# Optimization experiments

Hardware: AMD Instinct MI355X
Metric: run time of the kernel (lower is better)

The kernel has to match this reference:

```python
import jax, jax.numpy as jnp
import numpy as np

D_MODEL = 1024
N_HEADS = 16
BATCH = 2
SEQ = 2048


def get_freqs(seq, n_dim):
    # standard RoPE frequencies: [seq, n_dim//2]
    inv_freq = 1.0 / (10000.0 ** (jnp.arange(0, n_dim, 2, dtype=jnp.float32) / n_dim))
    return jnp.arange(seq, dtype=jnp.float32)[:, None] * inv_freq[None, :]


def rope(x, freqs):
    # x: [batch, seq, heads, n_dim]; half-split rotation convention
    half = x.shape[-1] // 2
    cos = jnp.cos(freqs)[None, :, None, :]  # [1, seq, 1, half]
    sin = jnp.sin(freqs)[None, :, None, :]
    x1, x2 = x[..., :half], x[..., half:]
    return jnp.concatenate([x1 * cos - x2 * sin, x1 * sin + x2 * cos], axis=-1)


def setup_inputs() -> dict:
    key = jax.random.key(0)
    ks = jax.random.split(key, 5)
    x = jax.random.normal(ks[0], (BATCH, SEQ, D_MODEL), dtype=jnp.float32)
    qw = jax.random.normal(ks[1], (D_MODEL, D_MODEL), dtype=jnp.float32)
    kw = jax.random.normal(ks[2], (D_MODEL, D_MODEL), dtype=jnp.float32)
    vw = jax.random.normal(ks[3], (D_MODEL, D_MODEL), dtype=jnp.float32)
    ow = jax.random.normal(ks[4], (D_MODEL, D_MODEL), dtype=jnp.float32)
    return {"x": x, "qw": qw, "kw": kw, "vw": vw, "ow": ow}


def reference(x, qw, kw, vw, ow):
    batch, seq, dim = x.shape
    n_heads = N_HEADS
    n_dim = dim // n_heads
    Q = (x @ qw).reshape(batch, seq, n_heads, n_dim)
    K = (x @ kw).reshape(batch, seq, n_heads, n_dim)
    V = (x @ vw).reshape(batch, seq, n_heads, n_dim)
    freqs = get_freqs(seq, n_dim)
    Q = rope(Q, freqs)
    K = rope(K, freqs)
    # NOTE: original divides by sqrt(d_model), not sqrt(head_dim)
    scale = 1.0 / jnp.sqrt(jnp.float32(dim))
    score = jnp.einsum('bqhd,bkhd->bhqk', Q, K) * scale
    weights = jax.nn.softmax(score.astype(jnp.float32), axis=-1)
    attn = jnp.einsum('bhqk,bkhd->bqhd', weights, V)
    merged = attn.reshape(batch, seq, dim)
    return merged @ ow
```

## Files before the change

kernel.cpp:

```cpp
#include <hip/hip_runtime.h>
#include <math.h>

#define DM 1024
#define NH 16
#define HD 64
#define BB 2
#define SS 2048
#define MM (BB*SS)

typedef unsigned short ushort_t;
typedef __attribute__((ext_vector_type(8))) short short8;
typedef __attribute__((ext_vector_type(4))) short short4_t;
typedef __attribute__((ext_vector_type(4))) float floatx4;

__device__ __forceinline__ ushort_t f2bf(float f) {
    unsigned int u = __float_as_uint(f);
    unsigned int r = u + 0x7fffu + ((u >> 16) & 1u);
    return (ushort_t)(r >> 16);
}
__device__ __forceinline__ float bf2f(ushort_t h) {
    return __uint_as_float(((unsigned int)h) << 16);
}

__device__ __forceinline__ void gl_lds16(const ushort_t* g, ushort_t* l) {
    __builtin_amdgcn_global_load_lds(
        (const __attribute__((address_space(1))) unsigned int*)g,
        (__attribute__((address_space(3))) unsigned int*)l, 16, 0, 0);
}

__global__ __launch_bounds__(256) void freq_kernel(float2* __restrict__ ct)
{
    const int idx = blockIdx.x * 256 + threadIdx.x;
    const int s = idx >> 5, j = idx & 31;
    const float invf = powf(10000.f, -(float)j * (1.f / 32.f));
    float sn, cs;
    sincosf((float)s * invf, &sn, &cs);
    ct[idx] = make_float2(cs, sn);
}

__global__ __launch_bounds__(256) void convert_x(const float* __restrict__ X,
                                                 ushort_t* __restrict__ Xh,
                                                 ushort_t* __restrict__ Xl)
{
    const size_t base = ((size_t)blockIdx.x * 256 + threadIdx.x) * 8;
    float v[8];
    *(float4*)&v[0] = *(const float4*)(X + base);
    *(float4*)&v[4] = *(const float4*)(X + base + 4);
    short8 h, l;
#pragma unroll
    for (int i = 0; i < 8; ++i) {
        const ushort_t hi = f2bf(v[i]);
        h[i] = (short)hi;
        l[i] = (short)f2bf(v[i] - bf2f(hi));
    }
    *(short8*)(Xh + base) = h;
    *(short8*)(Xl + base) = l;
}

template<int SPLIT>
__global__ __launch_bounds__(256) void convert_wt(const float* __restrict__ W,
                                                  ushort_t* __restrict__ Th,
                                                  ushort_t* __restrict__ Tl)
{
    __shared__ float tile[64][65];
    const int t  = threadIdx.x;
    const int kb = blockIdx.y * 64, nb = blockIdx.x * 64;
    const int r  = t >> 2;
    const int c0 = (t & 3) * 16;
#pragma unroll
    for (int i = 0; i < 4; ++i)
        *(float4*)&tile[r][c0 + 4 * i] = *(const float4*)(W + (size_t)(kb + r) * DM + nb + c0 + 4 * i);
    __syncthreads();
    ushort_t hi[16], lo[16];
#pragma unroll
    for (int i = 0; i < 16; ++i) {
        const float v = tile[c0 + i][r];
        hi[i] = f2bf(v);
        if (SPLIT) lo[i] = f2bf(v - bf2f(hi[i]));
    }
    const size_t dst = (size_t)(nb + r) * DM + kb + c0;
    *(short8*)(Th + dst)     = *(short8*)&hi[0];
    *(short8*)(Th + dst + 8) = *(short8*)&hi[8];
    if (SPLIT) {
        *(short8*)(Tl + dst)     = *(short8*)&lo[0];
        *(short8*)(Tl + dst + 8) = *(short8*)&lo[8];
    }
}

#define GTM 128

template<int UPR, int SH>
__device__ __forceinline__ void stage_tile(const ushort_t* __restrict__ G,
                                           ushort_t* L, int rows, int w, int lane)
{
    const int iters = rows * UPR / 256;
#pragma unroll
    for (int i = 0; i < iters; ++i) {
        const int p0 = (i * 4 + w) * 64;
        const int p  = p0 + lane;
        const int r  = p / UPR;
        const int u  = (p % UPR) ^ ((r >> SH) & (UPR - 1));
        gl_lds16(G + (size_t)r * DM + u * 8, L + (size_t)p0 * 8);
    }
}

template<int UPR, int SH>
__device__ __forceinline__ short8 frag(const ushort_t* L, int r, int u)
{
    const int uu = u ^ ((r >> SH) & (UPR - 1));
    return *(const short8*)&L[((size_t)r * UPR + uu) * 8];
}

template<int SPLIT, int OUT_MODE, int TN, int BK>
__global__ __launch_bounds__(256, 2) void gemm_mfma(
    const ushort_t* __restrict__ Ah, const ushort_t* __restrict__ Al,
    const ushort_t* __restrict__ Bh, const ushort_t* __restrict__ Bl,
    float* __restrict__ Cf, ushort_t* __restrict__ Cb, ushort_t* __restrict__ Cb2,
    const float2* __restrict__ CT)
{
    constexpr int UPR = BK / 8;
    constexpr int KC  = BK / 32;
    constexpr int NI  = TN / 32;
    constexpr int SH  = (UPR == 4) ? 1 : 0;

    __shared__ __align__(16) ushort_t AsH[GTM * BK];
    __shared__ __align__(16) ushort_t BsH[TN * BK];
    __shared__ __align__(16) ushort_t AsL[SPLIT ? GTM * BK : 8];
    __shared__ __align__(16) ushort_t BsL[SPLIT ? TN * BK : 8];
    __shared__ __align__(16) ushort_t Ts[(OUT_MODE == 2) ? 64 * 136 : 8];

    const int t    = threadIdx.x;
    const int w    = t >> 6;
    const int lane = t & 63;
    const int col  = lane & 15;
    const int quad = lane >> 4;
    const int wm   = w & 1;
    const int wn   = w >> 1;
    const int m0   = blockIdx.y * GTM;
    const int n0   = blockIdx.x * TN;

    floatx4 acc[4][NI];
#pragma unroll
    for (int mi = 0; mi < 4; ++mi)
#pragma unroll
        for (int ni = 0; ni < NI; ++ni) acc[mi][ni] = (floatx4){0.f, 0.f, 0.f, 0.f};

    for (int k0 = 0; k0 < DM; k0 += BK) {
        __syncthreads();
        stage_tile<UPR, SH>(Ah + (size_t)m0 * DM + k0, AsH, GTM, w, lane);
        if (SPLIT) stage_tile<UPR, SH>(Al + (size_t)m0 * DM + k0, AsL, GTM, w, lane);
        stage_tile<UPR, SH>(Bh + (size_t)n0 * DM + k0, BsH, TN, w, lane);
        if (SPLIT) stage_tile<UPR, SH>(Bl + (size_t)n0 * DM + k0, BsL, TN, w, lane);
        __syncthreads();

#pragma unroll
        for (int kc = 0; kc < KC; ++kc) {
            short8 ah[4], bh[NI];
            short8 al[SPLIT ? 4 : 1], bl[SPLIT ? NI : 1];
#pragma unroll
            for (int mi = 0; mi < 4; ++mi) {
                const int r = wm * 64 + mi * 16 + col;
                ah[mi] = frag<UPR, SH>(AsH, r, kc * 4 + quad);
                if (SPLIT) al[mi] = frag<UPR, SH>(AsL, r, kc * 4 + quad);
            }
#pragma unroll
            for (int ni = 0; ni < NI; ++ni) {
                const int r = wn * (TN / 2) + ni * 16 + col;
                bh[ni] = frag<UPR, SH>(BsH, r, kc * 4 + quad);
                if (SPLIT) bl[ni] = frag<UPR, SH>(BsL, r, kc * 4 + quad);
            }
#pragma unroll
            for (int mi = 0; mi < 4; ++mi)
#pragma unroll
                for (int ni = 0; ni < NI; ++ni) {
                    acc[mi][ni] = __builtin_amdgcn_mfma_f32_16x16x32_bf16(ah[mi], bh[ni], acc[mi][ni], 0, 0, 0);
                    if (SPLIT) {
                        acc[mi][ni] = __builtin_amdgcn_mfma_f32_16x16x32_bf16(al[mi], bh[ni], acc[mi][ni], 0, 0, 0);
                        acc[mi][ni] = __builtin_amdgcn_mfma_f32_16x16x32_bf16(ah[mi], bl[ni], acc[mi][ni], 0, 0, 0);
                    }
                }
        }
    }

    if constexpr (OUT_MODE == 0) {
#pragma unroll
        for (int mi = 0; mi < 4; ++mi)
#pragma unroll
            for (int ni = 0; ni < NI; ++ni)
#pragma unroll
                for (int r = 0; r < 4; ++r) {
                    const int m = m0 + wm * 64 + mi * 16 + quad * 4 + r;
                    const int n = n0 + wn * (TN / 2) + ni * 16 + col;
                    Cf[(size_t)m * DM + n] = acc[mi][ni][r];
                }
    }
    if constexpr (OUT_MODE == 2) {
#pragma unroll
        for (int mi = 0; mi < 4; ++mi)
#pragma unroll
            for (int ni = 0; ni < NI; ++ni) {
                const int nl = wn * (TN / 2) + ni * 16 + col;
                const int ml = wm * 64 + mi * 16 + quad * 4;
                short4_t pk;
#pragma unroll
                for (int r = 0; r < 4; ++r) pk[r] = (short)f2bf(acc[mi][ni][r]);
                *(short4_t*)&Ts[nl * 136 + ml] = pk;
            }
        __syncthreads();
        const int b = m0 >> 11, h = n0 >> 6;
        const int s0 = m0 & (SS - 1);
#pragma unroll
        for (int it = 0; it < 4; ++it) {
            const int idx = it * 256 + t;
            const int dr = idx >> 4, u = idx & 15;
            const short8 v = *(const short8*)&Ts[dr * 136 + u * 8];
            *(short8*)(Cb + ((size_t)((b << 4) + h) * HD + dr) * SS + s0 + u * 8) = v;
        }
    }
    if constexpr (OUT_MODE == 3) {
        const int tn = n0 >> 10;
#pragma unroll
        for (int mi = 0; mi < 4; ++mi)
#pragma unroll
            for (int ni = 0; ni < 2; ++ni)
#pragma unroll
                for (int r = 0; r < 4; ++r) {
                    const int m = m0 + wm * 64 + mi * 16 + quad * 4 + r;
                    const int n = n0 + wn * (TN / 2) + ni * 16 + col;
                    const int b = m >> 11, s = m & (SS - 1);
                    const int h = (n >> 6) & 15, d = n & 63;
                    const float2 cs = CT[(s << 5) + d];
                    const float x1 = acc[mi][ni][r];
                    const float x2 = acc[mi][ni + 2][r];
                    const float y1 = x1 * cs.x - x2 * cs.y;
                    const float y2 = x1 * cs.y + x2 * cs.x;
                    const size_t base = ((size_t)((b << 4) + h) * SS + s) * HD + d;
                    if (tn == 0) {
                        Cf[base]      = y1 * (1.f / 32.f);
                        Cf[base + 32] = y2 * (1.f / 32.f);
                    } else {
                        const ushort_t h1 = f2bf(y1), h2 = f2bf(y2);
                        Cb [base]      = h1;
                        Cb [base + 32] = h2;
                        Cb2[base]      = f2bf(y1 - bf2f(h1));
                        Cb2[base + 32] = f2bf(y2 - bf2f(h2));
                    }
                }
    }
}

__device__ __forceinline__ short8 afrag(const ushort_t* S, int r, int lu)
{
    return *(const short8*)&S[(size_t)(((r << 3) | (lu ^ (r & 7))) << 3)];
}

__global__ __launch_bounds__(256, 2) void attn_mfma2(
    const float* __restrict__ Qh, const ushort_t* __restrict__ Khi,
    const ushort_t* __restrict__ Klo, const ushort_t* __restrict__ Vt,
    ushort_t* __restrict__ Mgb)
{
    __shared__ __align__(16) ushort_t KhiS[64 * 64];
    __shared__ __align__(16) ushort_t KloS[64 * 64];
    __shared__ __align__(16) ushort_t VtS [64 * 64];
    __shared__ __align__(16) ushort_t PS  [128 * 64];

    const int t    = threadIdx.x;
    const int w    = t >> 6;
    const int lane = t & 63;
    const int col  = lane & 15;
    const int quad = lane >> 4;

    const int bh = blockIdx.y;
    const int q0 = blockIdx.x * 128;
    const float*    Qb  = Qh  + (size_t)bh * SS * HD;
    const ushort_t* KhB = Khi + (size_t)bh * SS * HD;
    const ushort_t* KlB = Klo + (size_t)bh * SS * HD;
    const ushort_t* VtB = Vt  + (size_t)bh * HD * SS;

    short8 qhi[2][2], qlo[2][2];
#pragma unroll
    for (int mi = 0; mi < 2; ++mi) {
#pragma unroll
        for (int ch = 0; ch < 2; ++ch) {
            const float* p = Qb + (size_t)(q0 + w * 32 + mi * 16 + col) * HD + ch * 32 + quad * 8;
            const float4 a = *(const float4*)p;
            const float4 b = *(const float4*)(p + 4);
            float v[8] = {a.x, a.y, a.z, a.w, b.x, b.y, b.z, b.w};
#pragma unroll
            for (int j = 0; j < 8; ++j) {
                const ushort_t h = f2bf(v[j]);
                qhi[mi][ch][j] = (short)h;
                qlo[mi][ch][j] = (short)f2bf(v[j] - bf2f(h));
            }
        }
    }

    floatx4 Oacc[2][4];
#pragma unroll
    for (int mi = 0; mi < 2; ++mi)
#pragma unroll
        for (int nt = 0; nt < 4; ++nt) Oacc[mi][nt] = (floatx4){0.f, 0.f, 0.f, 0.f};
    float mstat[2] = {-1e30f, -1e30f}, lstat[2] = {0.f, 0.f};

    for (int k0 = 0; k0 < SS; k0 += 64) {
        __syncthreads();
#pragma unroll
        for (int i = 0; i < 2; ++i) {
            const int p0 = w * 128 + i * 64;
            const int p  = p0 + lane;
            const int r  = p >> 3;
            const int gu = (p & 7) ^ (r & 7);
            gl_lds16(KhB + (size_t)(k0 + r) * HD + gu * 8, KhiS + (size_t)p0 * 8);
            gl_lds16(KlB + (size_t)(k0 + r) * HD + gu * 8, KloS + (size_t)p0 * 8);
            gl_lds16(VtB + (size_t)r * SS + k0 + gu * 8,   VtS  + (size_t)p0 * 8);
        }
        __syncthreads();

        floatx4 sc[4][2];
#pragma unroll
        for (int kt = 0; kt < 4; ++kt) {
            short8 kh[2], kl[2];
#pragma unroll
            for (int ch = 0; ch < 2; ++ch) {
                kh[ch] = afrag(KhiS, kt * 16 + col, ch * 4 + quad);
                kl[ch] = afrag(KloS, kt * 16 + col, ch * 4 + quad);
            }
#pragma unroll
            for (int mi = 0; mi < 2; ++mi) {
                floatx4 a = (floatx4){0.f, 0.f, 0.f, 0.f};
#pragma unroll
                for (int ch = 0; ch < 2; ++ch)
                    a = __builtin_amdgcn_mfma_f32_16x16x32_bf16(kh[ch], qhi[mi][ch], a, 0, 0, 0);
#pragma unroll
                for (int ch = 0; ch < 2; ++ch)
                    a = __builtin_amdgcn_mfma_f32_16x16x32_bf16(kh[ch], qlo[mi][ch], a, 0, 0, 0);
#pragma unroll
                for (int ch = 0; ch < 2; ++ch)
                    a = __builtin_amdgcn_mfma_f32_16x16x32_bf16(kl[ch], qhi[mi][ch], a, 0, 0, 0);
                sc[kt][mi] = a;
            }
        }

#pragma unroll
        for (int mi = 0; mi < 2; ++mi) {
            float mloc = -1e30f;
#pragma unroll
            for (int kt = 0; kt < 4; ++kt)
#pragma unroll
                for (int r = 0; r < 4; ++r) mloc = fmaxf(mloc, sc[kt][mi][r]);
            mloc = fmaxf(mloc, __shfl_xor(mloc, 16));
            mloc = fmaxf(mloc, __shfl_xor(mloc, 32));
            const float mnew  = fmaxf(mstat[mi], mloc);
            const float alpha = __expf(mstat[mi] - mnew);
            mstat[mi] = mnew;

            float psum = 0.f;
            const int qrow = w * 32 + mi * 16 + col;
#pragma unroll
            for (int kt = 0; kt < 4; ++kt) {
                short4_t pk;
#pragma unroll
                for (int r = 0; r < 4; ++r) {
                    const float p = __expf(sc[kt][mi][r] - mnew);
                    psum += p;
                    pk[r] = (short)f2bf(p);
                }
                const int u = (kt * 2 + (quad >> 1)) ^ (col & 7);
                *(short4_t*)&PS[(qrow << 6) + (u << 3) + ((quad & 1) << 2)] = pk;
            }
            psum += __shfl_xor(psum, 16);
            psum += __shfl_xor(psum, 32);
            lstat[mi] = lstat[mi] * alpha + psum;

            floatx4 alr;
#pragma unroll
            for (int r = 0; r < 4; ++r) alr[r] = __shfl(alpha, quad * 4 + r, 64);
#pragma unroll
            for (int nt = 0; nt < 4; ++nt)
#pragma unroll
                for (int r = 0; r < 4; ++r) Oacc[mi][nt][r] *= alr[r];
        }

        short8 pf[2][2];
#pragma unroll
        for (int mi = 0; mi < 2; ++mi)
#pragma unroll
            for (int ch = 0; ch < 2; ++ch)
                pf[mi][ch] = afrag(PS, w * 32 + mi * 16 + col, ch * 4 + quad);
#pragma unroll
        for (int nt = 0; nt < 4; ++nt) {
            short8 vf[2];
#pragma unroll
            for (int ch = 0; ch < 2; ++ch)
                vf[ch] = afrag(VtS, nt * 16 + col, ch * 4 + quad);
#pragma unroll
            for (int mi = 0; mi < 2; ++mi)
#pragma unroll
                for (int ch = 0; ch < 2; ++ch)
                    Oacc[mi][nt] = __builtin_amdgcn_mfma_f32_16x16x32_bf16(pf[mi][ch], vf[ch], Oacc[mi][nt], 0, 0, 0);
        }
    }

    const int b = bh >> 4, h = bh & 15;
#pragma unroll
    for (int mi = 0; mi < 2; ++mi) {
        floatx4 linv;
#pragma unroll
        for (int r = 0; r < 4; ++r) linv[r] = 1.f / __shfl(lstat[mi], quad * 4 + r, 64);
#pragma unroll
        for (int nt = 0; nt < 4; ++nt)
#pragma unroll
            for (int r = 0; r < 4; ++r) {
                const int srow = q0 + w * 32 + mi * 16 + quad * 4 + r;
                Mgb[(size_t)(b * SS + srow) * DM + h * HD + nt * 16 + col] =
                    f2bf(Oacc[mi][nt][r] * linv[r]);
            }
    }
}

extern "C" void kernel_launch(void* const* d_in, const int* in_sizes, int n_in,
                              void* d_out, int out_size, void* d_ws, size_t ws_size,
                              hipStream_t stream)
{
    const float* x  = (const float*)d_in[0];
    const float* qw = (const float*)d_in[1];
    const float* kw = (const float*)d_in[2];
    const float* vw = (const float*)d_in[3];
    const float* ow = (const float*)d_in[4];
    float* out = (float*)d_out;

    float*    Qh  = (float*)d_ws;
    ushort_t* Khi = (ushort_t*)(Qh + (size_t)MM * DM);
    ushort_t* Klo = Khi + (size_t)MM * DM;
    ushort_t* Vtb = Klo + (size_t)MM * DM;
    ushort_t* Mgb = Vtb + (size_t)MM * DM;
    ushort_t* xh  = Mgb + (size_t)MM * DM;
    ushort_t* xl  = xh  + (size_t)MM * DM;
    ushort_t* qkh = xl  + (size_t)MM * DM;
    ushort_t* qkl = qkh + (size_t)2048 * DM;
    ushort_t* vwt = qkl + (size_t)2048 * DM;
    ushort_t* owt = vwt + (size_t)DM * DM;
    float2*   ct  = (float2*)(owt + (size_t)DM * DM);

    freq_kernel<<<(SS * 32) / 256, 256, 0, stream>>>(ct);
    convert_x<<<(MM * DM) / (256 * 8), 256, 0, stream>>>(x, xh, xl);
    convert_wt<1><<<dim3(16, 16), 256, 0, stream>>>(qw, qkh, qkl);
    convert_wt<1><<<dim3(16, 16), 256, 0, stream>>>(kw, qkh + (size_t)DM * DM, qkl + (size_t)DM * DM);
    convert_wt<0><<<dim3(16, 16), 256, 0, stream>>>(vw, vwt, nullptr);
    convert_wt<0><<<dim3(16, 16), 256, 0, stream>>>(ow, owt, nullptr);

    gemm_mfma<1, 3, 128, 32><<<dim3(2048 / 128, MM / GTM), 256, 0, stream>>>(
        xh, xl, qkh, qkl, Qh, Khi, Klo, ct);
    gemm_mfma<0, 2, 64, 64><<<dim3(DM / 64, MM / GTM), 256, 0, stream>>>(
        xh, nullptr, vwt, nullptr, nullptr, Vtb, nullptr, nullptr);

    attn_mfma2<<<dim3(SS / 128, BB * NH), 256, 0, stream>>>(Qh, Khi, Klo, Vtb, Mgb);

    gemm_mfma<0, 0, 64, 64><<<dim3(DM / 64, MM / GTM), 256, 0, stream>>>(
        Mgb, nullptr, owt, nullptr, out, nullptr, nullptr, nullptr);
}
```

Measured before the change: 271.5 us.

## Double-buffer GEMM and attention LDS tiles, widen attention waves, merge weight conversions

Adds ping-pong LDS buffers to the GEMM and attention kernels. The load of the next K-tile is issued right after a single barrier, so it can overlap with the MFMA work on the current tile. The attention kernel now runs two waves per block, each covering 64 query rows, so more work shares each staged K/V tile, but fewer waves are resident. The four weight-conversion launches are merged into one 3D grid, and bf16 rounding is simplified from round-to-nearest-even to round-half-up, which slightly changes numerics.

```diff
diff --git a/kernel.cpp b/kernel.cpp
--- a/kernel.cpp
+++ b/kernel.cpp
@@ -14,9 +14,7 @@
 typedef __attribute__((ext_vector_type(4))) float floatx4;
 
 __device__ __forceinline__ ushort_t f2bf(float f) {
-    unsigned int u = __float_as_uint(f);
-    unsigned int r = u + 0x7fffu + ((u >> 16) & 1u);
-    return (ushort_t)(r >> 16);
+    return (ushort_t)((__float_as_uint(f) + 0x8000u) >> 16);
 }
 __device__ __forceinline__ float bf2f(ushort_t h) {
     return __uint_as_float(((unsigned int)h) << 16);
@@ -57,11 +55,21 @@
     *(short8*)(Xl + base) = l;
 }
 
-template<int SPLIT>
-__global__ __launch_bounds__(256) void convert_wt(const float* __restrict__ W,
-                                                  ushort_t* __restrict__ Th,
-                                                  ushort_t* __restrict__ Tl)
-{
+__global__ __launch_bounds__(256) void convert_w4(
+    const float* __restrict__ qw, const float* __restrict__ kw,
+    const float* __restrict__ vw, const float* __restrict__ ow,
+    ushort_t* __restrict__ qkh, ushort_t* __restrict__ qkl,
+    ushort_t* __restrict__ vwt, ushort_t* __restrict__ owt)
+{
+    const int which = blockIdx.z;
+    const float* W;
+    ushort_t *Th, *Tl = nullptr;
+    bool split = which < 2;
+    if (which == 0)      { W = qw; Th = qkh; Tl = qkl; }
+    else if (which == 1) { W = kw; Th = qkh + (size_t)DM * DM; Tl = qkl + (size_t)DM * DM; }
+    else if (which == 2) { W = vw; Th = vwt; }
+    else                 { W = ow; Th = owt; }
+
     __shared__ float tile[64][65];
     const int t  = threadIdx.x;
     const int kb = blockIdx.y * 64, nb = blockIdx.x * 64;
@@ -76,12 +84,12 @@
     for (int i = 0; i < 16; ++i) {
         const float v = tile[c0 + i][r];
         hi[i] = f2bf(v);
-        if (SPLIT) lo[i] = f2bf(v - bf2f(hi[i]));
+        lo[i] = f2bf(v - bf2f(hi[i]));
     }
     const size_t dst = (size_t)(nb + r) * DM + kb + c0;
     *(short8*)(Th + dst)     = *(short8*)&hi[0];
     *(short8*)(Th + dst + 8) = *(short8*)&hi[8];
-    if (SPLIT) {
+    if (split) {
         *(short8*)(Tl + dst)     = *(short8*)&lo[0];
         *(short8*)(Tl + dst + 8) = *(short8*)&lo[8];
     }
@@ -122,11 +130,12 @@
     constexpr int KC  = BK / 32;
     constexpr int NI  = TN / 32;
     constexpr int SH  = (UPR == 4) ? 1 : 0;
-
-    __shared__ __align__(16) ushort_t AsH[GTM * BK];
-    __shared__ __align__(16) ushort_t BsH[TN * BK];
-    __shared__ __align__(16) ushort_t AsL[SPLIT ? GTM * BK : 8];
-    __shared__ __align__(16) ushort_t BsL[SPLIT ? TN * BK : 8];
+    constexpr int NSTEP = DM / BK;
+
+    __shared__ __align__(16) ushort_t AsH[2][GTM * BK];
+    __shared__ __align__(16) ushort_t BsH[2][TN * BK];
+    __shared__ __align__(16) ushort_t AsL[2][SPLIT ? GTM * BK : 8];
+    __shared__ __align__(16) ushort_t BsL[2][SPLIT ? TN * BK : 8];
     __shared__ __align__(16) ushort_t Ts[(OUT_MODE == 2) ? 64 * 136 : 8];
 
     const int t    = threadIdx.x;
@@ -139,19 +148,32 @@
     const int m0   = blockIdx.y * GTM;
     const int n0   = blockIdx.x * TN;
 
+    const ushort_t* Abase = Ah + (size_t)m0 * DM;
+    const ushort_t* Bbase = Bh + (size_t)n0 * DM;
+    const ushort_t* AbaseL = SPLIT ? Al + (size_t)m0 * DM : nullptr;
+    const ushort_t* BbaseL = SPLIT ? Bl + (size_t)n0 * DM : nullptr;
+
     floatx4 acc[4][NI];
 #pragma unroll
     for (int mi = 0; mi < 4; ++mi)
 #pragma unroll
         for (int ni = 0; ni < NI; ++ni) acc[mi][ni] = (floatx4){0.f, 0.f, 0.f, 0.f};
 
-    for (int k0 = 0; k0 < DM; k0 += BK) {
+    stage_tile<UPR, SH>(Abase, AsH[0], GTM, w, lane);
+    if (SPLIT) stage_tile<UPR, SH>(AbaseL, AsL[0], GTM, w, lane);
+    stage_tile<UPR, SH>(Bbase, BsH[0], TN, w, lane);
+    if (SPLIT) stage_tile<UPR, SH>(BbaseL, BsL[0], TN, w, lane);
+
+    for (int ks = 0; ks < NSTEP; ++ks) {
+        const int cur = ks & 1;
         __syncthreads();
-        stage_tile<UPR, SH>(Ah + (size_t)m0 * DM + k0, AsH, GTM, w, lane);
-        if (SPLIT) stage_tile<UPR, SH>(Al + (size_t)m0 * DM + k0, AsL, GTM, w, lane);
-        stage_tile<UPR, SH>(Bh + (size_t)n0 * DM + k0, BsH, TN, w, lane);
-        if (SPLIT) stage_tile<UPR, SH>(Bl + (size_t)n0 * DM + k0, BsL, TN, w, lane);
-        __syncthreads();
+        if (ks + 1 < NSTEP) {
+            const int k1 = (ks + 1) * BK;
+            stage_tile<UPR, SH>(Abase + k1, AsH[cur ^ 1], GTM, w, lane);
+            if (SPLIT) stage_tile<UPR, SH>(AbaseL + k1, AsL[cur ^ 1], GTM, w, lane);
+            stage_tile<UPR, SH>(Bbase + k1, BsH[cur ^ 1], TN, w, lane);
+            if (SPLIT) stage_tile<UPR, SH>(BbaseL + k1, BsL[cur ^ 1], TN, w, lane);
+        }
 
 #pragma unroll
         for (int kc = 0; kc < KC; ++kc) {
@@ -160,14 +182,14 @@
 #pragma unroll
             for (int mi = 0; mi < 4; ++mi) {
                 const int r = wm * 64 + mi * 16 + col;
-                ah[mi] = frag<UPR, SH>(AsH, r, kc * 4 + quad);
-                if (SPLIT) al[mi] = frag<UPR, SH>(AsL, r, kc * 4 + quad);
+                ah[mi] = frag<UPR, SH>(AsH[cur], r, kc * 4 + quad);
+                if (SPLIT) al[mi] = frag<UPR, SH>(AsL[cur], r, kc * 4 + quad);
             }
 #pragma unroll
             for (int ni = 0; ni < NI; ++ni) {
                 const int r = wn * (TN / 2) + ni * 16 + col;
-                bh[ni] = frag<UPR, SH>(BsH, r, kc * 4 + quad);
-                if (SPLIT) bl[ni] = frag<UPR, SH>(BsL, r, kc * 4 + quad);
+                bh[ni] = frag<UPR, SH>(BsH[cur], r, kc * 4 + quad);
+                if (SPLIT) bl[ni] = frag<UPR, SH>(BsL[cur], r, kc * 4 + quad);
             }
 #pragma unroll
             for (int mi = 0; mi < 4; ++mi)
@@ -254,14 +276,32 @@
     return *(const short8*)&S[(size_t)(((r << 3) | (lu ^ (r & 7))) << 3)];
 }
 
-__global__ __launch_bounds__(256, 2) void attn_mfma2(
+__device__ __forceinline__ void attn_stage(const ushort_t* __restrict__ KhB,
+                                           const ushort_t* __restrict__ KlB,
+                                           const ushort_t* __restrict__ VtB,
+                                           int k0, ushort_t* dKh, ushort_t* dKl,
+                                           ushort_t* dVt, int w, int lane)
+{
+#pragma unroll
+    for (int i = 0; i < 4; ++i) {
+        const int p0 = (i * 2 + w) * 64;
+        const int p  = p0 + lane;
+        const int r  = p >> 3;
+        const int gu = (p & 7) ^ (r & 7);
+        gl_lds16(KhB + (size_t)(k0 + r) * HD + gu * 8, dKh + (size_t)p0 * 8);
+        gl_lds16(KlB + (size_t)(k0 + r) * HD + gu * 8, dKl + (size_t)p0 * 8);
+        gl_lds16(VtB + (size_t)r * SS + k0 + gu * 8,   dVt + (size_t)p0 * 8);
+    }
+}
+
+__global__ __launch_bounds__(128, 1) void attn_mfma3(
     const float* __restrict__ Qh, const ushort_t* __restrict__ Khi,
     const ushort_t* __restrict__ Klo, const ushort_t* __restrict__ Vt,
     ushort_t* __restrict__ Mgb)
 {
-    __shared__ __align__(16) ushort_t KhiS[64 * 64];
-    __shared__ __align__(16) ushort_t KloS[64 * 64];
-    __shared__ __align__(16) ushort_t VtS [64 * 64];
+    __shared__ __align__(16) ushort_t KhiS[2][64 * 64];
+    __shared__ __align__(16) ushort_t KloS[2][64 * 64];
+    __shared__ __align__(16) ushort_t VtS [2][64 * 64];
     __shared__ __align__(16) ushort_t PS  [128 * 64];
 
     const int t    = threadIdx.x;
@@ -277,12 +317,12 @@
     const ushort_t* KlB = Klo + (size_t)bh * SS * HD;
     const ushort_t* VtB = Vt  + (size_t)bh * HD * SS;
 
-    short8 qhi[2][2], qlo[2][2];
-#pragma unroll
-    for (int mi = 0; mi < 2; ++mi) {
+    short8 qhi[4][2], qlo[4][2];
+#pragma unroll
+    for (int mi = 0; mi < 4; ++mi) {
 #pragma unroll
         for (int ch = 0; ch < 2; ++ch) {
-            const float* p = Qb + (size_t)(q0 + w * 32 + mi * 16 + col) * HD + ch * 32 + quad * 8;
+            const float* p = Qb + (size_t)(q0 + w * 64 + mi * 16 + col) * HD + ch * 32 + quad * 8;
             const float4 a = *(const float4*)p;
             const float4 b = *(const float4*)(p + 4);
             float v[8] = {a.x, a.y, a.z, a.w, b.x, b.y, b.z, b.w};
@@ -295,38 +335,34 @@
         }
     }
 
-    floatx4 Oacc[2][4];
-#pragma unroll
-    for (int mi = 0; mi < 2; ++mi)
+    floatx4 Oacc[4][4];
+#pragma unroll
+    for (int mi = 0; mi < 4; ++mi)
 #pragma unroll
         for (int nt = 0; nt < 4; ++nt) Oacc[mi][nt] = (floatx4){0.f, 0.f, 0.f, 0.f};
-    float mstat[2] = {-1e30f, -1e30f}, lstat[2] = {0.f, 0.f};
-
-    for (int k0 = 0; k0 < SS; k0 += 64) {
+    float mstat[4] = {-1e30f, -1e30f, -1e30f, -1e30f};
+    float lstat[4] = {0.f, 0.f, 0.f, 0.f};
+
+    attn_stage(KhB, KlB, VtB, 0, KhiS[0], KloS[0], VtS[0], w, lane);
+
+    for (int kt0 = 0; kt0 < SS / 64; ++kt0) {
+        const int cur = kt0 & 1;
         __syncthreads();
-#pragma unroll
-        for (int i = 0; i < 2; ++i) {
-            const int p0 = w * 128 + i * 64;
-            const int p  = p0 + lane;
-            const int r  = p >> 3;
-            const int gu = (p & 7) ^ (r & 7);
-            gl_lds16(KhB + (size_t)(k0 + r) * HD + gu * 8, KhiS + (size_t)p0 * 8);
-            gl_lds16(KlB + (size_t)(k0 + r) * HD + gu * 8, KloS + (size_t)p0 * 8);
-            gl_lds16(VtB + (size_t)r * SS + k0 + gu * 8,   VtS  + (size_t)p0 * 8);
-        }
-        __syncthreads();
-
-        floatx4 sc[4][2];
+        if (kt0 + 1 < SS / 64)
+            attn_stage(KhB, KlB, VtB, (kt0 + 1) * 64,
+                       KhiS[cur ^ 1], KloS[cur ^ 1], VtS[cur ^ 1], w, lane);
+
+        floatx4 sc[4][4];
 #pragma unroll
         for (int kt = 0; kt < 4; ++kt) {
             short8 kh[2], kl[2];
 #pragma unroll
             for (int ch = 0; ch < 2; ++ch) {
-                kh[ch] = afrag(KhiS, kt * 16 + col, ch * 4 + quad);
-                kl[ch] = afrag(KloS, kt * 16 + col, ch * 4 + quad);
-            }
-#pragma unroll
-            for (int mi = 0; mi < 2; ++mi) {
+                kh[ch] = afrag(KhiS[cur], kt * 16 + col, ch * 4 + quad);
+                kl[ch] = afrag(KloS[cur], kt * 16 + col, ch * 4 + quad);
+            }
+#pragma unroll
+            for (int mi = 0; mi < 4; ++mi) {
                 floatx4 a = (floatx4){0.f, 0.f, 0.f, 0.f};
 #pragma unroll
                 for (int ch = 0; ch < 2; ++ch)
@@ -342,7 +378,7 @@
         }
 
 #pragma unroll
-        for (int mi = 0; mi < 2; ++mi) {
+        for (int mi = 0; mi < 4; ++mi) {
             float mloc = -1e30f;
 #pragma unroll
             for (int kt = 0; kt < 4; ++kt)
@@ -355,7 +391,7 @@
             mstat[mi] = mnew;
 
             float psum = 0.f;
-            const int qrow = w * 32 + mi * 16 + col;
+            const int qrow = w * 64 + mi * 16 + col;
 #pragma unroll
             for (int kt = 0; kt < 4; ++kt) {
                 short4_t pk;
@@ -381,20 +417,20 @@
                 for (int r = 0; r < 4; ++r) Oacc[mi][nt][r] *= alr[r];
         }
 
-        short8 pf[2][2];
-#pragma unroll
-        for (int mi = 0; mi < 2; ++mi)
+        short8 pf[4][2];
+#pragma unroll
+        for (int mi = 0; mi < 4; ++mi)
 #pragma unroll
             for (int ch = 0; ch < 2; ++ch)
-                pf[mi][ch] = afrag(PS, w * 32 + mi * 16 + col, ch * 4 + quad);
+                pf[mi][ch] = afrag(PS, w * 64 + mi * 16 + col, ch * 4 + quad);
 #pragma unroll
         for (int nt = 0; nt < 4; ++nt) {
             short8 vf[2];
 #pragma unroll
             for (int ch = 0; ch < 2; ++ch)
-                vf[ch] = afrag(VtS, nt * 16 + col, ch * 4 + quad);
-#pragma unroll
-            for (int mi = 0; mi < 2; ++mi)
+                vf[ch] = afrag(VtS[cur], nt * 16 + col, ch * 4 + quad);
+#pragma unroll
+            for (int mi = 0; mi < 4; ++mi)
 #pragma unroll
                 for (int ch = 0; ch < 2; ++ch)
                     Oacc[mi][nt] = __builtin_amdgcn_mfma_f32_16x16x32_bf16(pf[mi][ch], vf[ch], Oacc[mi][nt], 0, 0, 0);
@@ -403,7 +439,7 @@
 
     const int b = bh >> 4, h = bh & 15;
 #pragma unroll
-    for (int mi = 0; mi < 2; ++mi) {
+    for (int mi = 0; mi < 4; ++mi) {
         floatx4 linv;
 #pragma unroll
         for (int r = 0; r < 4; ++r) linv[r] = 1.f / __shfl(lstat[mi], quad * 4 + r, 64);
@@ -411,7 +447,7 @@
         for (int nt = 0; nt < 4; ++nt)
 #pragma unroll
             for (int r = 0; r < 4; ++r) {
-                const int srow = q0 + w * 32 + mi * 16 + quad * 4 + r;
+                const int srow = q0 + w * 64 + mi * 16 + quad * 4 + r;
                 Mgb[(size_t)(b * SS + srow) * DM + h * HD + nt * 16 + col] =
                     f2bf(Oacc[mi][nt][r] * linv[r]);
             }
@@ -444,17 +480,14 @@
 
     freq_kernel<<<(SS * 32) / 256, 256, 0, stream>>>(ct);
     convert_x<<<(MM * DM) / (256 * 8), 256, 0, stream>>>(x, xh, xl);
-    convert_wt<1><<<dim3(16, 16), 256, 0, stream>>>(qw, qkh, qkl);
-    convert_wt<1><<<dim3(16, 16), 256, 0, stream>>>(kw, qkh + (size_t)DM * DM, qkl + (size_t)DM * DM);
-    convert_wt<0><<<dim3(16, 16), 256, 0, stream>>>(vw, vwt, nullptr);
-    convert_wt<0><<<dim3(16, 16), 256, 0, stream>>>(ow, owt, nullptr);
+    convert_w4<<<dim3(16, 16, 4), 256, 0, stream>>>(qw, kw, vw, ow, qkh, qkl, vwt, owt);
 
     gemm_mfma<1, 3, 128, 32><<<dim3(2048 / 128, MM / GTM), 256, 0, stream>>>(
         xh, xl, qkh, qkl, Qh, Khi, Klo, ct);
     gemm_mfma<0, 2, 64, 64><<<dim3(DM / 64, MM / GTM), 256, 0, stream>>>(
         xh, nullptr, vwt, nullptr, nullptr, Vtb, nullptr, nullptr);
 
-    attn_mfma2<<<dim3(SS / 128, BB * NH), 256, 0, stream>>>(Qh, Khi, Klo, Vtb, Mgb);
+    attn_mfma3<<<dim3(SS / 128, BB * NH), 128, 0, stream>>>(Qh, Khi, Klo, Vtb, Mgb);
 
     gemm_mfma<0, 0, 64, 64><<<dim3(DM / 64, MM / GTM), 256, 0, stream>>>(
         Mgb, nullptr, owt, nullptr, out, nullptr, nullptr, nullptr);
```

Result: slower. 306.9 us (+13.0%).
